# Kernel optimization log

Measured on AMD Instinct MI355X. Metric: run time of the kernel, lower is better.

Reference implementation:

```python
import jax, jax.numpy as jnp
import numpy as np

H = 128

def _gru_layer(x_seq, Wih, Whh, bih, bhh):
    # x_seq: [B, T, I] -> hidden sequence [B, T, H]
    B, T, _ = x_seq.shape
    # precompute all input projections for the whole sequence (gate order: r, z, n)
    xi = jnp.einsum('bti,gi->btg', x_seq, Wih) + bih  # [B, T, 3H]
    def step(h, xt):
        gh = h @ Whh.T + bhh                           # [B, 3H]
        xr, xz, xn = xt[:, :H], xt[:, H:2*H], xt[:, 2*H:]
        hr, hz, hn = gh[:, :H], gh[:, H:2*H], gh[:, 2*H:]
        r = jax.nn.sigmoid(xr + hr)
        z = jax.nn.sigmoid(xz + hz)
        n = jnp.tanh(xn + r * hn)
        h_new = (1.0 - z) * n + z * h
        return h_new, h_new
    h0 = jnp.zeros((B, H), dtype=x_seq.dtype)
    _, hs = jax.lax.scan(step, h0, jnp.swapaxes(xi, 0, 1))  # hs: [T, B, H]
    return jnp.swapaxes(hs, 0, 1)


def setup_inputs() -> dict:
    key = jax.random.key(0)
    ks = jax.random.split(key, 12)
    s = 1.0 / np.sqrt(H)
    inp = {
        'x': jax.random.normal(ks[0], (512, 512, 5), dtype=jnp.float32),
        'Wih0': jax.random.uniform(ks[1], (3*H, 5), minval=-s, maxval=s, dtype=jnp.float32),
        'Whh0': jax.random.uniform(ks[2], (3*H, H), minval=-s, maxval=s, dtype=jnp.float32),
        'bih0': jax.random.uniform(ks[3], (3*H,), minval=-s, maxval=s, dtype=jnp.float32),
        'bhh0': jax.random.uniform(ks[4], (3*H,), minval=-s, maxval=s, dtype=jnp.float32),
        'Wih_rest': jax.random.uniform(ks[5], (3, 3*H, H), minval=-s, maxval=s, dtype=jnp.float32),
        'Whh_rest': jax.random.uniform(ks[6], (3, 3*H, H), minval=-s, maxval=s, dtype=jnp.float32),
        'bih_rest': jax.random.uniform(ks[7], (3, 3*H), minval=-s, maxval=s, dtype=jnp.float32),
        'bhh_rest': jax.random.uniform(ks[8], (3, 3*H), minval=-s, maxval=s, dtype=jnp.float32),
        'fc_w': jax.random.uniform(ks[9], (1, H), minval=-s, maxval=s, dtype=jnp.float32),
        'fc_b': jax.random.uniform(ks[10], (1,), minval=-s, maxval=s, dtype=jnp.float32),
    }
    return inp


def reference(x, Wih0, Whh0, bih0, bhh0, Wih_rest, Whh_rest, bih_rest, bhh_rest, fc_w, fc_b):
    # 4-layer GRU, batch_first, h0 = zeros; dropout in eval mode = identity.
    out = _gru_layer(x, Wih0, Whh0, bih0, bhh0)
    for l in range(3):
        out = _gru_layer(out, Wih_rest[l], Whh_rest[l], bih_rest[l], bhh_rest[l])
    last = out[:, -1, :]                     # [B, H]
    return last @ fc_w.T + fc_b              # [B, 1]
```

## Files before the change

kernel.cpp:

```cpp
#include <hip/hip_runtime.h>
#include <cmath>

#define HH   128
#define G3   384
#define TT   512
#define BTOT 512
#define BB   2
#define NBLK (BTOT / BB)
#define NTHR 512

__device__ __forceinline__ float sigmoidf_(float x) {
    return 1.0f / (1.0f + __expf(-x));
}

template <int INK, bool LAST>
__global__ __launch_bounds__(NTHR, 2) void gru_layer(
    const float* in, float* out,
    const float* __restrict__ Wih, const float* __restrict__ Whh,
    const float* __restrict__ bih, const float* __restrict__ bhh,
    const float* __restrict__ fcw, const float* __restrict__ fcb,
    float* __restrict__ fcout) {
    const int tid = threadIdx.x;
    const int kt  = tid & 3;
    const int gt  = tid >> 2;
    const int b0  = blockIdx.x * BB;

    __shared__ __align__(16) float s_h[2][BB][4][36];
    __shared__ __align__(16) float s_x[2][BB][(INK == 5) ? 8 : 144];

    float wh[3][32];
#pragma unroll
    for (int i = 0; i < 3; ++i) {
        const float* wr = Whh + (size_t)(i * HH + gt) * HH + kt * 32;
#pragma unroll
        for (int j = 0; j < 32; j += 4) {
            float4 v = *(const float4*)(wr + j);
            wh[i][j] = v.x; wh[i][j + 1] = v.y; wh[i][j + 2] = v.z; wh[i][j + 3] = v.w;
        }
    }
#pragma unroll
    for (int i = 0; i < 3; ++i)
#pragma unroll
        for (int j = 0; j < 32; ++j) asm volatile("" : "+v"(wh[i][j]));

    float wx[3][32];
    float wx5[3][5];
    if constexpr (INK == 128) {
#pragma unroll
        for (int i = 0; i < 3; ++i) {
            const float* wr = Wih + (size_t)(i * HH + gt) * HH + kt * 32;
#pragma unroll
            for (int j = 0; j < 32; j += 4) {
                float4 v = *(const float4*)(wr + j);
                wx[i][j] = v.x; wx[i][j + 1] = v.y; wx[i][j + 2] = v.z; wx[i][j + 3] = v.w;
            }
        }
#pragma unroll
        for (int i = 0; i < 3; ++i)
#pragma unroll
            for (int j = 0; j < 32; ++j) asm volatile("" : "+v"(wx[i][j]));
    } else {
#pragma unroll
        for (int i = 0; i < 3; ++i)
#pragma unroll
            for (int j = 0; j < 5; ++j) wx5[i][j] = Wih[(i * HH + gt) * 5 + j];
#pragma unroll
        for (int i = 0; i < 3; ++i)
#pragma unroll
            for (int j = 0; j < 5; ++j) asm volatile("" : "+v"(wx5[i][j]));
    }

    const float br  = bih[gt] + bhh[gt];
    const float bz  = bih[HH + gt] + bhh[HH + gt];
    const float bxn = bih[2 * HH + gt];
    const float bhn = bhh[2 * HH + gt];

    if (tid < BB * HH) {
        int bb = tid >> 7, j = tid & (HH - 1);
        s_h[0][bb][j >> 5][j & 31] = 0.0f;
    }
    if constexpr (INK == 5) {
        if (tid < BB * 5) {
            int bb = tid / 5, k = tid % 5;
            s_x[0][bb][k] = in[((size_t)(b0 + bb) * TT + 0) * 5 + k];
        }
    } else {
        if (tid < 64) {
            int row = tid >> 5, f = (tid & 31) * 4;
            float4 v = *(const float4*)&in[((size_t)(b0 + row) * TT + 0) * HH + f];
            *(float4*)&s_x[0][row][(f >> 5) * 36 + (f & 31)] = v;
        }
    }
    __syncthreads();

    for (int t = 0; t < TT; ++t) {
        const int cur = t & 1, nxt = cur ^ 1;

        float4 xs4 = make_float4(0.f, 0.f, 0.f, 0.f);
        float  xs1 = 0.f;
        if constexpr (INK == 5) {
            if (tid < BB * 5 && t + 1 < TT) {
                int bb = tid / 5, k = tid % 5;
                xs1 = in[((size_t)(b0 + bb) * TT + (t + 1)) * 5 + k];
            }
        } else {
            if (tid < 64 && t + 1 < TT) {
                int row = tid >> 5, f = (tid & 31) * 4;
                xs4 = *(const float4*)&in[((size_t)(b0 + row) * TT + (t + 1)) * HH + f];
            }
        }

        float acc[BB][4];
#pragma unroll
        for (int bb = 0; bb < BB; ++bb) {
            acc[bb][0] = 0.f; acc[bb][1] = 0.f; acc[bb][2] = 0.f; acc[bb][3] = 0.f;
        }
#pragma unroll
        for (int bb = 0; bb < BB; ++bb) {
            const float* hp = &s_h[cur][bb][kt][0];
            const float* xp = &s_x[cur][bb][(INK == 5) ? 0 : kt * 36];
#pragma unroll
            for (int jj = 0; jj < 32; jj += 4) {
                float4 hu = *(const float4*)(hp + jj);
                acc[bb][0] = fmaf(wh[0][jj], hu.x, acc[bb][0]);
                acc[bb][0] = fmaf(wh[0][jj+1], hu.y, acc[bb][0]);
                acc[bb][0] = fmaf(wh[0][jj+2], hu.z, acc[bb][0]);
                acc[bb][0] = fmaf(wh[0][jj+3], hu.w, acc[bb][0]);
                acc[bb][1] = fmaf(wh[1][jj], hu.x, acc[bb][1]);
                acc[bb][1] = fmaf(wh[1][jj+1], hu.y, acc[bb][1]);
                acc[bb][1] = fmaf(wh[1][jj+2], hu.z, acc[bb][1]);
                acc[bb][1] = fmaf(wh[1][jj+3], hu.w, acc[bb][1]);
                acc[bb][3] = fmaf(wh[2][jj], hu.x, acc[bb][3]);
                acc[bb][3] = fmaf(wh[2][jj+1], hu.y, acc[bb][3]);
                acc[bb][3] = fmaf(wh[2][jj+2], hu.z, acc[bb][3]);
                acc[bb][3] = fmaf(wh[2][jj+3], hu.w, acc[bb][3]);
                if constexpr (INK == 128) {
                    float4 xu = *(const float4*)(xp + jj);
                    acc[bb][0] = fmaf(wx[0][jj], xu.x, acc[bb][0]);
                    acc[bb][0] = fmaf(wx[0][jj+1], xu.y, acc[bb][0]);
                    acc[bb][0] = fmaf(wx[0][jj+2], xu.z, acc[bb][0]);
                    acc[bb][0] = fmaf(wx[0][jj+3], xu.w, acc[bb][0]);
                    acc[bb][1] = fmaf(wx[1][jj], xu.x, acc[bb][1]);
                    acc[bb][1] = fmaf(wx[1][jj+1], xu.y, acc[bb][1]);
                    acc[bb][1] = fmaf(wx[1][jj+2], xu.z, acc[bb][1]);
                    acc[bb][1] = fmaf(wx[1][jj+3], xu.w, acc[bb][1]);
                    acc[bb][2] = fmaf(wx[2][jj], xu.x, acc[bb][2]);
                    acc[bb][2] = fmaf(wx[2][jj+1], xu.y, acc[bb][2]);
                    acc[bb][2] = fmaf(wx[2][jj+2], xu.z, acc[bb][2]);
                    acc[bb][2] = fmaf(wx[2][jj+3], xu.w, acc[bb][2]);
                }
            }
        }
#pragma unroll
        for (int bb = 0; bb < BB; ++bb)
#pragma unroll
            for (int g = 0; g < 4; ++g) {
                if (INK == 5 && g == 2) continue;
                acc[bb][g] += __shfl_xor(acc[bb][g], 1, 64);
                acc[bb][g] += __shfl_xor(acc[bb][g], 2, 64);
            }

        if (kt < 2) {
            const int bb = kt;
            float cr  = (kt == 0) ? acc[0][0] : acc[1][0];
            float cz  = (kt == 0) ? acc[0][1] : acc[1][1];
            float cnx = (kt == 0) ? acc[0][2] : acc[1][2];
            float cnh = (kt == 0) ? acc[0][3] : acc[1][3];
            if constexpr (INK == 5) {
                float x0 = s_x[cur][bb][0], x1 = s_x[cur][bb][1], x2 = s_x[cur][bb][2];
                float x3 = s_x[cur][bb][3], x4 = s_x[cur][bb][4];
                cr += wx5[0][0]*x0 + wx5[0][1]*x1 + wx5[0][2]*x2 + wx5[0][3]*x3 + wx5[0][4]*x4;
                cz += wx5[1][0]*x0 + wx5[1][1]*x1 + wx5[1][2]*x2 + wx5[1][3]*x3 + wx5[1][4]*x4;
                cnx = wx5[2][0]*x0 + wx5[2][1]*x1 + wx5[2][2]*x2 + wx5[2][3]*x3 + wx5[2][4]*x4;
            }
            float r = sigmoidf_(cr + br);
            float z = sigmoidf_(cz + bz);
            float n = tanhf(cnx + bxn + r * (cnh + bhn));
            float hp = s_h[cur][bb][gt >> 5][gt & 31];
            float hv = (1.0f - z) * n + z * hp;
            s_h[nxt][bb][gt >> 5][gt & 31] = hv;
            if (!LAST) out[((size_t)(b0 + bb) * TT + t) * HH + gt] = hv;
        }

        if constexpr (INK == 5) {
            if (tid < BB * 5 && t + 1 < TT) {
                int bb = tid / 5, k = tid % 5;
                s_x[nxt][bb][k] = xs1;
            }
        } else {
            if (tid < 64 && t + 1 < TT) {
                int row = tid >> 5, f = (tid & 31) * 4;
                *(float4*)&s_x[nxt][row][(f >> 5) * 36 + (f & 31)] = xs4;
            }
        }
        __syncthreads();
    }

    if (LAST) {
        if (tid < 128) {
            int bb = tid >> 6, l = tid & 63;
            float h0 = s_h[0][bb][l >> 5][l & 31];
            float h1 = s_h[0][bb][(l >> 5) + 2][l & 31];
            float s = h0 * fcw[l] + h1 * fcw[l + 64];
#pragma unroll
            for (int m = 32; m >= 1; m >>= 1) s += __shfl_xor(s, m, 64);
            if (l == 0) fcout[b0 + bb] = s + fcb[0];
        }
    }
}

extern "C" void kernel_launch(void* const* d_in, const int* in_sizes, int n_in,
                              void* d_out, int out_size, void* d_ws, size_t ws_size,
                              hipStream_t stream) {
    const float* x    = (const float*)d_in[0];
    const float* Wih0 = (const float*)d_in[1];
    const float* Whh0 = (const float*)d_in[2];
    const float* bih0 = (const float*)d_in[3];
    const float* bhh0 = (const float*)d_in[4];
    const float* WihR = (const float*)d_in[5];
    const float* WhhR = (const float*)d_in[6];
    const float* bihR = (const float*)d_in[7];
    const float* bhhR = (const float*)d_in[8];
    const float* fcw  = (const float*)d_in[9];
    const float* fcb  = (const float*)d_in[10];

    float* buf = (float*)d_ws;

    gru_layer<5, false><<<NBLK, NTHR, 0, stream>>>(x, buf, Wih0, Whh0, bih0, bhh0,
                                                   nullptr, nullptr, nullptr);
    gru_layer<128, false><<<NBLK, NTHR, 0, stream>>>(buf, buf, WihR, WhhR, bihR, bhhR,
                                                     nullptr, nullptr, nullptr);
    gru_layer<128, false><<<NBLK, NTHR, 0, stream>>>(buf, buf, WihR + G3 * HH, WhhR + G3 * HH,
                                                     bihR + G3, bhhR + G3,
                                                     nullptr, nullptr, nullptr);
    gru_layer<128, true><<<NBLK, NTHR, 0, stream>>>(buf, buf, WihR + 2 * G3 * HH,
                                                    WhhR + 2 * G3 * HH, bihR + 2 * G3,
                                                    bhhR + 2 * G3, fcw, fcb, (float*)d_out);
}
```

Baseline: 3.641 ms.

## Hoist input projections into separate batched GEMM ahead of GRU recurrence

Layers 2-4 now compute the input-to-hidden projection for all timesteps with a separate tiled GEMM kernel into a workspace buffer. The recurrent kernel then only does the hidden-state matvec and reads the precomputed gates, prefetched two steps ahead. This removes half the per-step serial FMA work and the Wih register footprint from the latency-bound recurrence, at the cost of extra global traffic for the xi buffer and extra launches. It also swaps tanhf for an exp-based tanh, uses a lighter LDS-only barrier, and unrolls the time loop by two. The original fused path is kept as a fallback when the workspace is too small.

```diff
diff --git a/kernel.cpp b/kernel.cpp
--- a/kernel.cpp
+++ b/kernel.cpp
@@ -12,9 +12,234 @@
 __device__ __forceinline__ float sigmoidf_(float x) {
     return 1.0f / (1.0f + __expf(-x));
 }
+__device__ __forceinline__ float tanhf_(float x) {
+    float e = __expf(2.0f * x);
+    return 1.0f - 2.0f / (e + 1.0f);
+}
+__device__ __forceinline__ void lds_barrier() {
+    asm volatile("s_waitcnt lgkmcnt(0)" ::: "memory");
+    __builtin_amdgcn_s_barrier();
+}
+
+__global__ __launch_bounds__(512, 4) void xi_gemm(
+    const float* __restrict__ hin, const float* __restrict__ Wih,
+    float* __restrict__ xi) {
+    const int tid = threadIdx.x;
+    const int g   = tid & 127;
+    const int tq  = tid >> 7;
+    const size_t tok0 = (size_t)blockIdx.x * 32;
+    __shared__ __align__(16) float s_in[32][HH];
+#pragma unroll
+    for (int r = 0; r < 2; ++r) {
+        int f4 = tid * 2 + r;
+        int tk = f4 >> 5, k4 = (f4 & 31) << 2;
+        *(float4*)&s_in[tk][k4] = *(const float4*)&hin[(tok0 + tk) * HH + k4];
+    }
+    __syncthreads();
+    float acc[3][8];
+#pragma unroll
+    for (int i = 0; i < 3; ++i)
+#pragma unroll
+        for (int t = 0; t < 8; ++t) acc[i][t] = 0.0f;
+    const float* w0 = Wih + (size_t)g * HH;
+    const float* w1 = Wih + (size_t)(HH + g) * HH;
+    const float* w2 = Wih + (size_t)(2 * HH + g) * HH;
+#pragma unroll 2
+    for (int kc = 0; kc < 32; ++kc) {
+        float4 wa = *(const float4*)(w0 + kc * 4);
+        float4 wb = *(const float4*)(w1 + kc * 4);
+        float4 wc = *(const float4*)(w2 + kc * 4);
+#pragma unroll
+        for (int t = 0; t < 8; ++t) {
+            float4 sv = *(const float4*)&s_in[tq * 8 + t][kc * 4];
+            acc[0][t] = fmaf(wa.x, sv.x, acc[0][t]); acc[0][t] = fmaf(wa.y, sv.y, acc[0][t]);
+            acc[0][t] = fmaf(wa.z, sv.z, acc[0][t]); acc[0][t] = fmaf(wa.w, sv.w, acc[0][t]);
+            acc[1][t] = fmaf(wb.x, sv.x, acc[1][t]); acc[1][t] = fmaf(wb.y, sv.y, acc[1][t]);
+            acc[1][t] = fmaf(wb.z, sv.z, acc[1][t]); acc[1][t] = fmaf(wb.w, sv.w, acc[1][t]);
+            acc[2][t] = fmaf(wc.x, sv.x, acc[2][t]); acc[2][t] = fmaf(wc.y, sv.y, acc[2][t]);
+            acc[2][t] = fmaf(wc.z, sv.z, acc[2][t]); acc[2][t] = fmaf(wc.w, sv.w, acc[2][t]);
+        }
+    }
+#pragma unroll
+    for (int i = 0; i < 3; ++i)
+#pragma unroll
+        for (int t = 0; t < 8; ++t)
+            xi[(tok0 + tq * 8 + t) * G3 + i * HH + g] = acc[i][t];
+}
+
+template <bool FIRST, bool LAST>
+__global__ __launch_bounds__(NTHR, 2) void gru_rec(
+    const float* __restrict__ xin,
+    float* __restrict__ hout,
+    const float* __restrict__ Wih5, const float* __restrict__ Whh,
+    const float* __restrict__ bih, const float* __restrict__ bhh,
+    const float* __restrict__ fcw, const float* __restrict__ fcb,
+    float* __restrict__ fcout) {
+    const int tid = threadIdx.x;
+    const int kt  = tid & 3;
+    const int gt  = tid >> 2;
+    const int b0  = blockIdx.x * BB;
+
+    __shared__ __align__(16) float s_h[2][BB][4][36];
+    __shared__ __align__(16) float s_xi[2][BB][G3];
+    __shared__ float s_x5[2][BB][8];
+
+    float wh[3][32];
+#pragma unroll
+    for (int i = 0; i < 3; ++i) {
+        const float* wr = Whh + (size_t)(i * HH + gt) * HH + kt * 32;
+#pragma unroll
+        for (int j = 0; j < 32; j += 4) {
+            float4 v = *(const float4*)(wr + j);
+            wh[i][j] = v.x; wh[i][j + 1] = v.y; wh[i][j + 2] = v.z; wh[i][j + 3] = v.w;
+        }
+    }
+#pragma unroll
+    for (int i = 0; i < 3; ++i)
+#pragma unroll
+        for (int j = 0; j < 32; ++j) asm volatile("" : "+v"(wh[i][j]));
+
+    float wx5[3][5];
+    if constexpr (FIRST) {
+#pragma unroll
+        for (int i = 0; i < 3; ++i)
+#pragma unroll
+            for (int j = 0; j < 5; ++j) wx5[i][j] = Wih5[(i * HH + gt) * 5 + j];
+    }
+
+    const float br  = bih[gt] + bhh[gt];
+    const float bz  = bih[HH + gt] + bhh[HH + gt];
+    const float bxn = bih[2 * HH + gt];
+    const float bhn = bhh[2 * HH + gt];
+
+    if (tid < BB * HH) {
+        int bb = tid >> 7, j = tid & (HH - 1);
+        s_h[0][bb][j >> 5][j & 31] = 0.0f;
+    }
+
+    float4 P0 = make_float4(0.f, 0.f, 0.f, 0.f), P1 = P0;
+    float  q0 = 0.f, q1 = 0.f;
+    if constexpr (!FIRST) {
+        if (tid < 192) {
+            int bb = tid / 96, e = tid % 96;
+            const float* base = xin + ((size_t)(b0 + bb) * TT) * G3 + e * 4;
+            float4 v = *(const float4*)(base);
+            P0 = *(const float4*)(base + (size_t)G3);
+            P1 = *(const float4*)(base + (size_t)2 * G3);
+            *(float4*)&s_xi[0][bb][e * 4] = v;
+        }
+    } else {
+        if (tid < 16) {
+            int bb = tid >> 3, k = tid & 7;
+            if (k < 5) {
+                const float* base = xin + ((size_t)(b0 + bb) * TT) * 5 + k;
+                float v = base[0];
+                q0 = base[5];
+                q1 = base[10];
+                s_x5[0][bb][k] = v;
+            }
+        }
+    }
+    __syncthreads();
+
+#define REC_STEP(CUR, T, PV, QV)                                                   \
+    {                                                                              \
+                  \
+        if constexpr (!FIRST) {                                                    \
+            if (tid < 192) {                                                       \
+                int bb = tid / 96, e = tid % 96;                                   \
+                *(float4*)&s_xi[CUR ^ 1][bb][e * 4] = PV;                          \
+                int tl = (T) + 3 < TT ? (T) + 3 : TT - 1;                          \
+                PV = *(const float4*)(xin + ((size_t)(b0 + bb) * TT + tl) * G3 + e * 4); \
+            }                                                                      \
+        } else {                                                                   \
+            if (tid < 16) {                                                        \
+                int bb = tid >> 3, k = tid & 7;                                    \
+                if (k < 5) {                                                       \
+                    s_x5[CUR ^ 1][bb][k] = QV;                                     \
+                    int tl = (T) + 3 < TT ? (T) + 3 : TT - 1;                      \
+                    QV = xin[((size_t)(b0 + bb) * TT + tl) * 5 + k];               \
+                }                                                                  \
+            }                                                                      \
+        }                                                                          \
+        float a00 = 0.f, a01 = 0.f, a02 = 0.f, a10 = 0.f, a11 = 0.f, a12 = 0.f;    \
+        const float* hp0 = &s_h[CUR][0][kt][0];                                    \
+        const float* hp1 = &s_h[CUR][1][kt][0];                                    \
+        _Pragma("unroll")                                                          \
+        for (int jj = 0; jj < 32; jj += 4) {                                       \
+            float4 u = *(const float4*)(hp0 + jj);                                 \
+            float4 v = *(const float4*)(hp1 + jj);                                 \
+            a00 = fmaf(wh[0][jj], u.x, a00); a00 = fmaf(wh[0][jj+1], u.y, a00);    \
+            a00 = fmaf(wh[0][jj+2], u.z, a00); a00 = fmaf(wh[0][jj+3], u.w, a00);  \
+            a01 = fmaf(wh[1][jj], u.x, a01); a01 = fmaf(wh[1][jj+1], u.y, a01);    \
+            a01 = fmaf(wh[1][jj+2], u.z, a01); a01 = fmaf(wh[1][jj+3], u.w, a01);  \
+            a02 = fmaf(wh[2][jj], u.x, a02); a02 = fmaf(wh[2][jj+1], u.y, a02);    \
+            a02 = fmaf(wh[2][jj+2], u.z, a02); a02 = fmaf(wh[2][jj+3], u.w, a02);  \
+            a10 = fmaf(wh[0][jj], v.x, a10); a10 = fmaf(wh[0][jj+1], v.y, a10);    \
+            a10 = fmaf(wh[0][jj+2], v.z, a10); a10 = fmaf(wh[0][jj+3], v.w, a10);  \
+            a11 = fmaf(wh[1][jj], v.x, a11); a11 = fmaf(wh[1][jj+1], v.y, a11);    \
+            a11 = fmaf(wh[1][jj+2], v.z, a11); a11 = fmaf(wh[1][jj+3], v.w, a11);  \
+            a12 = fmaf(wh[2][jj], v.x, a12); a12 = fmaf(wh[2][jj+1], v.y, a12);    \
+            a12 = fmaf(wh[2][jj+2], v.z, a12); a12 = fmaf(wh[2][jj+3], v.w, a12);  \
+        }                                                                          \
+        a00 += __shfl_xor(a00, 1, 64); a00 += __shfl_xor(a00, 2, 64);              \
+        a01 += __shfl_xor(a01, 1, 64); a01 += __shfl_xor(a01, 2, 64);              \
+        a02 += __shfl_xor(a02, 1, 64); a02 += __shfl_xor(a02, 2, 64);              \
+        a10 += __shfl_xor(a10, 1, 64); a10 += __shfl_xor(a10, 2, 64);              \
+        a11 += __shfl_xor(a11, 1, 64); a11 += __shfl_xor(a11, 2, 64);              \
+        a12 += __shfl_xor(a12, 1, 64); a12 += __shfl_xor(a12, 2, 64);              \
+        if (kt < 2) {                                                              \
+            const int bb = kt;                                                     \
+            float cr  = (kt == 0) ? a00 : a10;                                     \
+            float cz  = (kt == 0) ? a01 : a11;                                     \
+            float cnh = (kt == 0) ? a02 : a12;                                     \
+            float xr, xz, xn;                                                      \
+            if constexpr (!FIRST) {                                                \
+                xr = s_xi[CUR][bb][gt];                                            \
+                xz = s_xi[CUR][bb][HH + gt];                                       \
+                xn = s_xi[CUR][bb][2 * HH + gt];                                   \
+            } else {                                                               \
+                float x0 = s_x5[CUR][bb][0], x1 = s_x5[CUR][bb][1];                \
+                float x2 = s_x5[CUR][bb][2], x3 = s_x5[CUR][bb][3];                \
+                float x4 = s_x5[CUR][bb][4];                                       \
+                xr = wx5[0][0]*x0 + wx5[0][1]*x1 + wx5[0][2]*x2 + wx5[0][3]*x3 + wx5[0][4]*x4; \
+                xz = wx5[1][0]*x0 + wx5[1][1]*x1 + wx5[1][2]*x2 + wx5[1][3]*x3 + wx5[1][4]*x4; \
+                xn = wx5[2][0]*x0 + wx5[2][1]*x1 + wx5[2][2]*x2 + wx5[2][3]*x3 + wx5[2][4]*x4; \
+            }                                                                      \
+            float r = sigmoidf_(xr + cr + br);                                     \
+            float z = sigmoidf_(xz + cz + bz);                                     \
+            float n = tanhf_(xn + bxn + r * (cnh + bhn));                          \
+            float hp = s_h[CUR][bb][gt >> 5][gt & 31];                             \
+            float hv = (1.0f - z) * n + z * hp;                                    \
+            s_h[CUR ^ 1][bb][gt >> 5][gt & 31] = hv;                               \
+            if constexpr (!LAST)                                                   \
+                hout[((size_t)(b0 + bb) * TT + (T)) * HH + gt] = hv;               \
+        }                                                                          \
+        lds_barrier();                                                             \
+    }
+
+#pragma unroll 1
+    for (int t = 0; t < TT; t += 2) {
+        REC_STEP(0, t, P0, q0)
+        REC_STEP(1, t + 1, P1, q1)
+    }
+#undef REC_STEP
+
+    if constexpr (LAST) {
+        if (tid < 128) {
+            int bb = tid >> 6, l = tid & 63;
+            float h0 = s_h[0][bb][l >> 5][l & 31];
+            float h1 = s_h[0][bb][(l >> 5) + 2][l & 31];
+            float s = h0 * fcw[l] + h1 * fcw[l + 64];
+#pragma unroll
+            for (int m = 32; m >= 1; m >>= 1) s += __shfl_xor(s, m, 64);
+            if (l == 0) fcout[b0 + bb] = s + fcb[0];
+        }
+    }
+}
 
 template <int INK, bool LAST>
-__global__ __launch_bounds__(NTHR, 2) void gru_layer(
+__global__ __launch_bounds__(NTHR, 2) void gru_fused(
     const float* in, float* out,
     const float* __restrict__ Wih, const float* __restrict__ Whh,
     const float* __restrict__ bih, const float* __restrict__ bhh,
@@ -24,10 +249,8 @@
     const int kt  = tid & 3;
     const int gt  = tid >> 2;
     const int b0  = blockIdx.x * BB;
-
     __shared__ __align__(16) float s_h[2][BB][4][36];
     __shared__ __align__(16) float s_x[2][BB][(INK == 5) ? 8 : 144];
-
     float wh[3][32];
 #pragma unroll
     for (int i = 0; i < 3; ++i) {
@@ -42,9 +265,7 @@
     for (int i = 0; i < 3; ++i)
 #pragma unroll
         for (int j = 0; j < 32; ++j) asm volatile("" : "+v"(wh[i][j]));
-
-    float wx[3][32];
-    float wx5[3][5];
+    float wx[3][32]; float wx5[3][5];
     if constexpr (INK == 128) {
 #pragma unroll
         for (int i = 0; i < 3; ++i) {
@@ -64,17 +285,11 @@
         for (int i = 0; i < 3; ++i)
 #pragma unroll
             for (int j = 0; j < 5; ++j) wx5[i][j] = Wih[(i * HH + gt) * 5 + j];
-#pragma unroll
-        for (int i = 0; i < 3; ++i)
-#pragma unroll
-            for (int j = 0; j < 5; ++j) asm volatile("" : "+v"(wx5[i][j]));
-    }
-
+    }
     const float br  = bih[gt] + bhh[gt];
     const float bz  = bih[HH + gt] + bhh[HH + gt];
     const float bxn = bih[2 * HH + gt];
     const float bhn = bhh[2 * HH + gt];
-
     if (tid < BB * HH) {
         int bb = tid >> 7, j = tid & (HH - 1);
         s_h[0][bb][j >> 5][j & 31] = 0.0f;
@@ -82,20 +297,18 @@
     if constexpr (INK == 5) {
         if (tid < BB * 5) {
             int bb = tid / 5, k = tid % 5;
-            s_x[0][bb][k] = in[((size_t)(b0 + bb) * TT + 0) * 5 + k];
+            s_x[0][bb][k] = in[((size_t)(b0 + bb) * TT) * 5 + k];
         }
     } else {
         if (tid < 64) {
             int row = tid >> 5, f = (tid & 31) * 4;
-            float4 v = *(const float4*)&in[((size_t)(b0 + row) * TT + 0) * HH + f];
+            float4 v = *(const float4*)&in[((size_t)(b0 + row) * TT) * HH + f];
             *(float4*)&s_x[0][row][(f >> 5) * 36 + (f & 31)] = v;
         }
     }
     __syncthreads();
-
     for (int t = 0; t < TT; ++t) {
         const int cur = t & 1, nxt = cur ^ 1;
-
         float4 xs4 = make_float4(0.f, 0.f, 0.f, 0.f);
         float  xs1 = 0.f;
         if constexpr (INK == 5) {
@@ -109,7 +322,6 @@
                 xs4 = *(const float4*)&in[((size_t)(b0 + row) * TT + (t + 1)) * HH + f];
             }
         }
-
         float acc[BB][4];
 #pragma unroll
         for (int bb = 0; bb < BB; ++bb) {
@@ -159,7 +371,6 @@
                 acc[bb][g] += __shfl_xor(acc[bb][g], 1, 64);
                 acc[bb][g] += __shfl_xor(acc[bb][g], 2, 64);
             }
-
         if (kt < 2) {
             const int bb = kt;
             float cr  = (kt == 0) ? acc[0][0] : acc[1][0];
@@ -175,13 +386,12 @@
             }
             float r = sigmoidf_(cr + br);
             float z = sigmoidf_(cz + bz);
-            float n = tanhf(cnx + bxn + r * (cnh + bhn));
+            float n = tanhf_(cnx + bxn + r * (cnh + bhn));
             float hp = s_h[cur][bb][gt >> 5][gt & 31];
             float hv = (1.0f - z) * n + z * hp;
             s_h[nxt][bb][gt >> 5][gt & 31] = hv;
             if (!LAST) out[((size_t)(b0 + bb) * TT + t) * HH + gt] = hv;
         }
-
         if constexpr (INK == 5) {
             if (tid < BB * 5 && t + 1 < TT) {
                 int bb = tid / 5, k = tid % 5;
@@ -195,7 +405,6 @@
         }
         __syncthreads();
     }
-
     if (LAST) {
         if (tid < 128) {
             int bb = tid >> 6, l = tid & 63;
@@ -224,16 +433,36 @@
     const float* fcw  = (const float*)d_in[9];
     const float* fcb  = (const float*)d_in[10];
 
+    const size_t BUF_B = (size_t)BTOT * TT * HH * 4;
+    const size_t XI_B  = (size_t)BTOT * TT * G3 * 4;
     float* buf = (float*)d_ws;
 
-    gru_layer<5, false><<<NBLK, NTHR, 0, stream>>>(x, buf, Wih0, Whh0, bih0, bhh0,
-                                                   nullptr, nullptr, nullptr);
-    gru_layer<128, false><<<NBLK, NTHR, 0, stream>>>(buf, buf, WihR, WhhR, bihR, bhhR,
-                                                     nullptr, nullptr, nullptr);
-    gru_layer<128, false><<<NBLK, NTHR, 0, stream>>>(buf, buf, WihR + G3 * HH, WhhR + G3 * HH,
-                                                     bihR + G3, bhhR + G3,
-                                                     nullptr, nullptr, nullptr);
-    gru_layer<128, true><<<NBLK, NTHR, 0, stream>>>(buf, buf, WihR + 2 * G3 * HH,
-                                                    WhhR + 2 * G3 * HH, bihR + 2 * G3,
-                                                    bhhR + 2 * G3, fcw, fcb, (float*)d_out);
-}
+    if (ws_size >= BUF_B + XI_B) {
+        float* xi = (float*)((char*)d_ws + BUF_B);
+        const int GB = (BTOT * TT) / 32;
+        gru_rec<true, false><<<NBLK, NTHR, 0, stream>>>(x, buf, Wih0, Whh0, bih0, bhh0,
+                                                        nullptr, nullptr, nullptr);
+        for (int l = 0; l < 3; ++l) {
+            xi_gemm<<<GB, 512, 0, stream>>>(buf, WihR + (size_t)l * G3 * HH, xi);
+            if (l < 2)
+                gru_rec<false, false><<<NBLK, NTHR, 0, stream>>>(
+                    xi, buf, nullptr, WhhR + (size_t)l * G3 * HH, bihR + l * G3,
+                    bhhR + l * G3, nullptr, nullptr, nullptr);
+            else
+                gru_rec<false, true><<<NBLK, NTHR, 0, stream>>>(
+                    xi, buf, nullptr, WhhR + (size_t)l * G3 * HH, bihR + l * G3,
+                    bhhR + l * G3, fcw, fcb, (float*)d_out);
+        }
+    } else {
+        gru_fused<5, false><<<NBLK, NTHR, 0, stream>>>(x, buf, Wih0, Whh0, bih0, bhh0,
+                                                       nullptr, nullptr, nullptr);
+        gru_fused<128, false><<<NBLK, NTHR, 0, stream>>>(buf, buf, WihR, WhhR, bihR, bhhR,
+                                                         nullptr, nullptr, nullptr);
+        gru_fused<128, false><<<NBLK, NTHR, 0, stream>>>(buf, buf, WihR + G3 * HH,
+                                                         WhhR + G3 * HH, bihR + G3,
+                                                         bhhR + G3, nullptr, nullptr, nullptr);
+        gru_fused<128, true><<<NBLK, NTHR, 0, stream>>>(buf, buf, WihR + 2 * G3 * HH,
+                                                        WhhR + 2 * G3 * HH, bihR + 2 * G3,
+                                                        bhhR + 2 * G3, fcw, fcb, (float*)d_out);
+    }
+}
```

After: 3.312 ms (median of 5 runs). 1.1x faster.
